# Kernel optimization log

Measured on AMD Instinct MI355X. Metric: run time of the kernel, lower is better.

Reference implementation:

```python
import jax, jax.numpy as jnp
import numpy as np

N = 50000      # nodes
E = 800000     # edges (before self loops)
G = 64         # graphs in batch
IN = 128       # in_features
HID = 64       # hidden_dim per head
HEADS = 4
NC = 2         # num_classes
SLOPE = 0.2    # PyG GATConv negative_slope default


def setup_inputs() -> dict:
    key = jax.random.key(0)
    ks = jax.random.split(key, 16)
    s = 0.1
    HC = HID * HEADS
    inp = {
        "x": jax.random.normal(ks[0], (N, IN), jnp.float32),
        "edge_index": jax.random.randint(ks[1], (2, E), 0, N, jnp.int64),
        "batch": jnp.sort(jax.random.randint(ks[2], (N,), 0, G, jnp.int64)),
        # GATConv 1: lin weight [H*C, IN], att vecs [H, C], bias [H*C]
        "W1": jax.random.normal(ks[3], (HC, IN), jnp.float32) * s,
        "as1": jax.random.normal(ks[4], (HEADS, HID), jnp.float32) * s,
        "ad1": jax.random.normal(ks[5], (HEADS, HID), jnp.float32) * s,
        "b1": jnp.zeros((HC,), jnp.float32),
        # GATConv 2
        "W2": jax.random.normal(ks[6], (HC, HC), jnp.float32) * s,
        "as2": jax.random.normal(ks[7], (HEADS, HID), jnp.float32) * s,
        "ad2": jax.random.normal(ks[8], (HEADS, HID), jnp.float32) * s,
        "b2": jnp.zeros((HC,), jnp.float32),
        # GATConv 3
        "W3": jax.random.normal(ks[9], (HC, HC), jnp.float32) * s,
        "as3": jax.random.normal(ks[10], (HEADS, HID), jnp.float32) * s,
        "ad3": jax.random.normal(ks[11], (HEADS, HID), jnp.float32) * s,
        "b3": jnp.zeros((HC,), jnp.float32),
        # MLP head
        "fc1_w": jax.random.normal(ks[12], (HID, HC), jnp.float32) * s,
        "fc1_b": jnp.zeros((HID,), jnp.float32),
        "fc2_w": jax.random.normal(ks[13], (NC, HID), jnp.float32) * s,
        "fc2_b": jnp.zeros((NC,), jnp.float32),
    }
    return inp


def gat_conv(x, src, dst, W, a_src, a_dst, b):
    """PyG-style GATConv (concat=True, self loops already in src/dst)."""
    n = x.shape[0]
    h = (x @ W.T).reshape(n, HEADS, HID)            # [N,H,C]
    al_s = jnp.sum(h * a_src[None], axis=-1)        # [N,H]
    al_d = jnp.sum(h * a_dst[None], axis=-1)        # [N,H]
    e = jax.nn.leaky_relu(al_s[src] + al_d[dst], SLOPE)  # [Et,H]
    # segment softmax over edges grouped by destination node
    m = jax.ops.segment_max(e, dst, num_segments=n)      # [N,H]
    ex = jnp.exp(e - m[dst])
    den = jax.ops.segment_sum(ex, dst, num_segments=n)
    alpha = ex / (den[dst] + 1e-16)                      # [Et,H]
    out = jax.ops.segment_sum(h[src] * alpha[:, :, None], dst, num_segments=n)
    return out.reshape(n, HEADS * HID) + b


def reference(x, edge_index, batch, W1, as1, ad1, b1, W2, as2, ad2, b2,
              W3, as3, ad3, b3, fc1_w, fc1_b, fc2_w, fc2_b):
    loops = jnp.arange(N, dtype=edge_index.dtype)
    src = jnp.concatenate([edge_index[0], loops])   # add_self_loops=True
    dst = jnp.concatenate([edge_index[1], loops])

    h = jax.nn.relu(gat_conv(x, src, dst, W1, as1, ad1, b1))
    h = jax.nn.relu(gat_conv(h, src, dst, W2, as2, ad2, b2))
    h = gat_conv(h, src, dst, W3, as3, ad3, b3)

    # global_mean_pool over batch vector
    sums = jax.ops.segment_sum(h, batch, num_segments=G)          # [G,H*C]
    cnts = jax.ops.segment_sum(jnp.ones((N,), h.dtype), batch, num_segments=G)
    pooled = sums / jnp.maximum(cnts, 1.0)[:, None]

    z = jax.nn.relu(pooled @ fc1_w.T + fc1_b)
    return z @ fc2_w.T + fc2_b                                    # [G,NC]
```

## Files before the change

### kernel.cpp

```cpp
#include <hip/hip_runtime.h>
#include <hip/hip_bf16.h>

#define N_NODES 50000
#define E_EDGES 800000
#define ET (E_EDGES + N_NODES)
#define G_GRAPHS 64
#define IN_F 128
#define HID 64
#define HEADS 4
#define HC (HID * HEADS)
#define NC 2
#define SLOPE 0.2f
#define L2E 1.4426950408889634f

typedef float f32x4 __attribute__((ext_vector_type(4)));
typedef __bf16 bf16x8 __attribute__((ext_vector_type(8)));
typedef unsigned short us8 __attribute__((ext_vector_type(8)));
typedef unsigned short us4 __attribute__((ext_vector_type(4)));
typedef _Float16 h16x4 __attribute__((ext_vector_type(4)));

#define MFMA16(a, b, c) \
  __builtin_amdgcn_mfma_f32_16x16x32_bf16(__builtin_bit_cast(bf16x8, (a)), \
                                          __builtin_bit_cast(bf16x8, (b)), (c), 0, 0, 0)

typedef __attribute__((address_space(1))) void gvoid;
typedef __attribute__((address_space(3))) void lvoid;
#define GLD16(g, l) \
  __builtin_amdgcn_global_load_lds((gvoid*)(g), (lvoid*)(l), 16, 0, 0)

__device__ inline unsigned short f2bf_rne(float f) {
  unsigned u = __builtin_bit_cast(unsigned, f);
  u += 0x7fffu + ((u >> 16) & 1u);
  return (unsigned short)(u >> 16);
}
__device__ inline float bf2f(unsigned short h) {
  unsigned u = ((unsigned)h) << 16;
  return __builtin_bit_cast(float, u);
}


__device__ inline void split4(const float* __restrict__ in, unsigned short* __restrict__ hi,
                              unsigned short* __restrict__ lo, int i) {
  float4 v = *(const float4*)&in[i];
  float f[4] = {v.x, v.y, v.z, v.w};
  us4 h, l;
#pragma unroll
  for (int j = 0; j < 4; j++) {
    unsigned short hb = f2bf_rne(f[j]);
    h[j] = hb;
    l[j] = f2bf_rne(f[j] - bf2f(hb));
  }
  *(us4*)&hi[i] = h;
  *(us4*)&lo[i] = l;
}

#define QX (N_NODES * IN_F / 4)
#define QW1 (HC * IN_F / 4)
#define QW2 (HC * HC / 4)
#define QTOT (QX + QW1 + 2 * QW2)

__global__ __launch_bounds__(256) void split_all_kernel(
    const float* __restrict__ x, const float* __restrict__ W1,
    const float* __restrict__ W2, const float* __restrict__ W3,
    unsigned short* __restrict__ xhi,
    unsigned short* __restrict__ w1h, unsigned short* __restrict__ w1l,
    unsigned short* __restrict__ w2h, unsigned short* __restrict__ w2l,
    unsigned short* __restrict__ w3h, unsigned short* __restrict__ w3l) {
  int q = blockIdx.x * 256 + threadIdx.x;
  if (q < QX) {
    int i = q * 4;
    float4 v = *(const float4*)&x[i];
    float f[4] = {v.x, v.y, v.z, v.w};
    us4 h;
#pragma unroll
    for (int j = 0; j < 4; j++) h[j] = f2bf_rne(f[j]);
    *(us4*)&xhi[i] = h;
  } else if (q < QX + QW1) {
    split4(W1, w1h, w1l, (q - QX) * 4);
  } else if (q < QX + QW1 + QW2) {
    split4(W2, w2h, w2l, (q - QX - QW1) * 4);
  } else {
    split4(W3, w3h, w3l, (q - QX - QW1 - QW2) * 4);
  }
}


__global__ void count_kernel(const int* __restrict__ ei, int* __restrict__ cnt) {
  int e = blockIdx.x * blockDim.x + threadIdx.x;
  if (e >= ET) return;
  int dst = (e < E_EDGES) ? ei[E_EDGES + e] : (e - E_EDGES);
  atomicAdd(&cnt[dst], 1);
}

#define SCAN_BLOCKS ((N_NODES + 255) / 256)

__global__ __launch_bounds__(256) void scan1_kernel(const int* __restrict__ cnt,
                                                    int* __restrict__ incl_buf,
                                                    int* __restrict__ partial) {
  __shared__ int ws[4];
  int tid = threadIdx.x, b = blockIdx.x;
  int wave = tid >> 6, lane = tid & 63;
  int i = b * 256 + tid;
  int v = (i < N_NODES) ? cnt[i] : 0;
  int x = v;
#pragma unroll
  for (int off = 1; off < 64; off <<= 1) {
    int t = __shfl_up(x, off, 64);
    if (lane >= off) x += t;
  }
  if (lane == 63) ws[wave] = x;
  __syncthreads();
  if (tid == 0) {
    int s = 0;
#pragma unroll
    for (int w = 0; w < 4; w++) { int t = ws[w]; ws[w] = s; s += t; }
    partial[b] = s;
  }
  __syncthreads();
  if (i < N_NODES) incl_buf[i] = x + ws[wave];
}

__global__ __launch_bounds__(256) void scan2_kernel(int* __restrict__ partial) {
  __shared__ int ws[4];
  int tid = threadIdx.x;
  int wave = tid >> 6, lane = tid & 63;
  int v = (tid < SCAN_BLOCKS) ? partial[tid] : 0;
  int x = v;
#pragma unroll
  for (int off = 1; off < 64; off <<= 1) {
    int t = __shfl_up(x, off, 64);
    if (lane >= off) x += t;
  }
  if (lane == 63) ws[wave] = x;
  __syncthreads();
  if (tid == 0) {
    int s = 0;
#pragma unroll
    for (int w = 0; w < 4; w++) { int t = ws[w]; ws[w] = s; s += t; }
  }
  __syncthreads();
  partial[tid] = x + ws[wave] - v;
}

__global__ __launch_bounds__(256) void scan3_kernel(const int* __restrict__ cnt,
                                                    int* __restrict__ incl_buf,
                                                    const int* __restrict__ partial,
                                                    int* __restrict__ rowptr,
                                                    int* __restrict__ cursor) {
  int tid = threadIdx.x, b = blockIdx.x;
  int i = b * 256 + tid;
  if (i >= N_NODES) return;
  int incl = incl_buf[i] + partial[b];
  rowptr[i + 1] = incl;
  cursor[i] = incl - cnt[i];
  if (i == 0) rowptr[0] = 0;
}

__global__ void scatter_kernel(const int* __restrict__ ei, int* __restrict__ cursor,
                               int* __restrict__ csr_src) {
  int e = blockIdx.x * blockDim.x + threadIdx.x;
  if (e >= ET) return;
  int src, dst;
  if (e < E_EDGES) { src = ei[e]; dst = ei[E_EDGES + e]; }
  else { src = e - E_EDGES; dst = src; }
  int pos = atomicAdd(&cursor[dst], 1);
  csr_src[pos] = src;
}


template <int K>
__global__ __launch_bounds__(256) void mfma_gemm_kernel(
    const unsigned short* __restrict__ A,
    const unsigned short* __restrict__ Whi, const unsigned short* __restrict__ Wlo,
    const float* __restrict__ a_s, const float* __restrict__ a_d,
    _Float16* __restrict__ hbuf16, float* __restrict__ als, float* __restrict__ ald) {
  __shared__ unsigned short As[4 * 64 * 8];
  __shared__ unsigned short Bs[2 * 4 * 256 * 8];

  int t = threadIdx.x;
  int mt = blockIdx.x;
  int w = t >> 6, lane = t & 63, lr = lane & 15, kg = lane >> 4;

  f32x4 acc[4][4];
#pragma unroll
  for (int m = 0; m < 4; m++)
#pragma unroll
    for (int nf = 0; nf < 4; nf++) {
      f32x4 z = {0.f, 0.f, 0.f, 0.f};
      acc[m][nf] = z;
    }

  for (int k0 = 0; k0 < K; k0 += 32) {
    __syncthreads();
#pragma unroll
    for (int j = 0; j < 8; j++) {
      int c = w * 512 + j * 64 + lane;
      int plane = c >> 10;
      int bkg = (c >> 8) & 3;
      int n = c & 255;
      const unsigned short* gsrc =
          (plane ? Wlo : Whi) + (size_t)n * K + k0 + bkg * 8;
      GLD16(gsrc, &Bs[(size_t)(w * 512 + j * 64) * 8]);
    }
    {
      const unsigned short* gsrc = A + (size_t)(mt * 64 + lane) * K + k0 + w * 8;
      GLD16(gsrc, &As[(size_t)(w * 64) * 8]);
    }
    __syncthreads();

    us8 bh[4], bl[4];
#pragma unroll
    for (int nf = 0; nf < 4; nf++) {
      int n = w * 64 + nf * 16 + lr;
      bh[nf] = *(us8*)&Bs[(size_t)(kg * 256 + n) * 8];
      bl[nf] = *(us8*)&Bs[(size_t)((4 + kg) * 256 + n) * 8];
    }
#pragma unroll
    for (int m = 0; m < 4; m++) {
      int row = m * 16 + lr;
      us8 ah = *(us8*)&As[(size_t)(kg * 64 + row) * 8];
#pragma unroll
      for (int nf = 0; nf < 4; nf++) {
        acc[m][nf] = MFMA16(ah, bh[nf], acc[m][nf]);
        acc[m][nf] = MFMA16(ah, bl[nf], acc[m][nf]);
      }
    }
  }

  int head = w;
  float asv[4], adv[4];
#pragma unroll
  for (int nf = 0; nf < 4; nf++) {
    asv[nf] = a_s[head * HID + nf * 16 + lr];
    adv[nf] = a_d[head * HID + nf * 16 + lr];
  }
#pragma unroll
  for (int m = 0; m < 4; m++) {
#pragma unroll
    for (int r = 0; r < 4; r++) {
      int grow = mt * 64 + m * 16 + kg * 4 + r;
      float ps = 0.f, pd = 0.f;
#pragma unroll
      for (int nf = 0; nf < 4; nf++) {
        float v = acc[m][nf][r];
        ps += v * asv[nf];
        pd += v * adv[nf];
        if (grow < N_NODES)
          hbuf16[(size_t)grow * HC + head * 64 + nf * 16 + lr] = (_Float16)v;
      }
#pragma unroll
      for (int msk = 1; msk < 16; msk <<= 1) {
        ps += __shfl_xor(ps, msk, 64);
        pd += __shfl_xor(pd, msk, 64);
      }
      if (lr == 0 && grow < N_NODES) {
        als[grow * HEADS + head] = ps * L2E;
        ald[grow * HEADS + head] = pd * L2E;
      }
    }
  }
}


template <int MODE>
__global__ __launch_bounds__(256) void agg_kernel(
    const _Float16* __restrict__ hbuf16, const float* __restrict__ alsE,
    const float* __restrict__ aldE, const int* __restrict__ rowptr,
    const int* __restrict__ csr_src, const float* __restrict__ bias,
    unsigned short* __restrict__ ohi, float* __restrict__ pooled,
    const int* __restrict__ batch) {
  int wave = threadIdx.x >> 6;
  int lane = threadIdx.x & 63;
  int v0 = blockIdx.x * 8 + wave * 2;
  int v1 = v0 + 1;
  int head = lane >> 4;
  float ald0 = aldE[(unsigned)v0 * HEADS + head];
  float ald1 = aldE[(unsigned)v1 * HEADS + head];
  int beg0 = rowptr[v0], n0 = rowptr[v0 + 1] - beg0;
  int beg1 = rowptr[v1], n1 = rowptr[v1 + 1] - beg1;
  int n = max(n0, n1);

  float den0 = 0.f, den1 = 0.f;
  f32x4 acc0 = {0.f, 0.f, 0.f, 0.f};
  f32x4 acc1 = {0.f, 0.f, 0.f, 0.f};
  const _Float16* hp = hbuf16 + (lane << 2);
#pragma unroll 2
  for (int i = 0; i < n; i++) {
    int s0 = csr_src[beg0 + min(i, n0 - 1)];
    int s1 = csr_src[beg1 + min(i, n1 - 1)];
    float a0 = alsE[(unsigned)s0 * HEADS + head] + ald0;
    float a1 = alsE[(unsigned)s1 * HEADS + head] + ald1;
    a0 = fmaxf(a0, SLOPE * a0);
    a1 = fmaxf(a1, SLOPE * a1);
    float ex0 = (i < n0) ? __builtin_amdgcn_exp2f(a0) : 0.f;
    float ex1 = (i < n1) ? __builtin_amdgcn_exp2f(a1) : 0.f;
    h16x4 h0 = *(const h16x4*)(hp + ((unsigned)s0 << 8));
    h16x4 h1 = *(const h16x4*)(hp + ((unsigned)s1 << 8));
    den0 += ex0; den1 += ex1;
    acc0[0] += (float)h0[0] * ex0; acc0[1] += (float)h0[1] * ex0;
    acc0[2] += (float)h0[2] * ex0; acc0[3] += (float)h0[3] * ex0;
    acc1[0] += (float)h1[0] * ex1; acc1[1] += (float)h1[1] * ex1;
    acc1[2] += (float)h1[2] * ex1; acc1[3] += (float)h1[3] * ex1;
  }
  float inv0 = 1.0f / (den0 + 1e-16f);
  float inv1 = 1.0f / (den1 + 1e-16f);
  float4 bv = *(const float4*)&bias[lane * 4];
  float o0[4], o1[4];
  o0[0] = acc0[0] * inv0 + bv.x; o0[1] = acc0[1] * inv0 + bv.y;
  o0[2] = acc0[2] * inv0 + bv.z; o0[3] = acc0[3] * inv0 + bv.w;
  o1[0] = acc1[0] * inv1 + bv.x; o1[1] = acc1[1] * inv1 + bv.y;
  o1[2] = acc1[2] * inv1 + bv.z; o1[3] = acc1[3] * inv1 + bv.w;

  if (MODE == 0) {
    us4 h0, h1;
#pragma unroll
    for (int j = 0; j < 4; j++) {
      h0[j] = f2bf_rne(fmaxf(o0[j], 0.f));
      h1[j] = f2bf_rne(fmaxf(o1[j], 0.f));
    }
    *(us4*)&ohi[(size_t)v0 * HC + lane * 4] = h0;
    *(us4*)&ohi[(size_t)v1 * HC + lane * 4] = h1;
  } else {
    __shared__ float pacc[8][HC];
    __shared__ int pg[8];
    f32x4 ov0 = {o0[0], o0[1], o0[2], o0[3]};
    f32x4 ov1 = {o1[0], o1[1], o1[2], o1[3]};
    *(f32x4*)&pacc[wave * 2][lane * 4] = ov0;
    *(f32x4*)&pacc[wave * 2 + 1][lane * 4] = ov1;
    if (lane == 0) {
      pg[wave * 2] = batch[v0];
      pg[wave * 2 + 1] = batch[v1];
    }
    __syncthreads();
    int c = threadIdx.x;
    float s = pacc[0][c];
    int gcur = pg[0];
#pragma unroll
    for (int wv = 1; wv < 8; wv++) {
      if (pg[wv] != gcur) {
        atomicAdd(&pooled[gcur * HC + c], s);
        s = 0.f;
        gcur = pg[wv];
      }
      s += pacc[wv][c];
    }
    atomicAdd(&pooled[gcur * HC + c], s);
  }
}


__global__ __launch_bounds__(64) void mlp_kernel(const float* __restrict__ pooled_sum,
                                                 const int* __restrict__ batch,
                                                 const float* __restrict__ w1,
                                                 const float* __restrict__ b1,
                                                 const float* __restrict__ w2,
                                                 const float* __restrict__ b2,
                                                 float* __restrict__ out) {
  int g = blockIdx.x;
  int j = threadIdx.x;
  int lo = 0, hi = N_NODES;
  while (lo < hi) { int mid = (lo + hi) >> 1; if (batch[mid] < g) lo = mid + 1; else hi = mid; }
  int start = lo;
  hi = N_NODES;
  while (lo < hi) { int mid = (lo + hi) >> 1; if (batch[mid] < g + 1) lo = mid + 1; else hi = mid; }
  float invc = 1.0f / fmaxf((float)(lo - start), 1.0f);
  __shared__ float z[HID];
  float acc = 0.f;
  for (int k = 0; k < HC; k++) acc += pooled_sum[g * HC + k] * w1[j * HC + k];
  z[j] = fmaxf(acc * invc + b1[j], 0.f);
  __syncthreads();
  if (j < NC) {
    float o = b2[j];
    for (int k = 0; k < HID; k++) o += z[k] * w2[j * HID + k];
    out[g * NC + j] = o;
  }
}


extern "C" void kernel_launch(void* const* d_in, const int* in_sizes, int n_in,
                              void* d_out, int out_size, void* d_ws, size_t ws_size,
                              hipStream_t stream) {
  const float* x    = (const float*)d_in[0];
  const int*   ei   = (const int*)d_in[1];
  const int*   batch= (const int*)d_in[2];
  const float* W1   = (const float*)d_in[3];
  const float* as1  = (const float*)d_in[4];
  const float* ad1  = (const float*)d_in[5];
  const float* b1   = (const float*)d_in[6];
  const float* W2   = (const float*)d_in[7];
  const float* as2  = (const float*)d_in[8];
  const float* ad2  = (const float*)d_in[9];
  const float* b2   = (const float*)d_in[10];
  const float* W3   = (const float*)d_in[11];
  const float* as3  = (const float*)d_in[12];
  const float* ad3  = (const float*)d_in[13];
  const float* b3   = (const float*)d_in[14];
  const float* fc1w = (const float*)d_in[15];
  const float* fc1b = (const float*)d_in[16];
  const float* fc2w = (const float*)d_in[17];
  const float* fc2b = (const float*)d_in[18];
  float* out = (float*)d_out;

  char* ws = (char*)d_ws;
  size_t off = 0;
  _Float16* hbuf16 = (_Float16*)(ws + off); off += (size_t)N_NODES * HC * 2;
  unsigned short* ahi = (unsigned short*)(ws + off); off += (size_t)N_NODES * HC * 2;
  unsigned short* xhi = (unsigned short*)(ws + off); off += (size_t)N_NODES * IN_F * 2;
  unsigned short* w1h = (unsigned short*)(ws + off); off += (size_t)HC * IN_F * 2;
  unsigned short* w1l = (unsigned short*)(ws + off); off += (size_t)HC * IN_F * 2;
  unsigned short* w2h = (unsigned short*)(ws + off); off += (size_t)HC * HC * 2;
  unsigned short* w2l = (unsigned short*)(ws + off); off += (size_t)HC * HC * 2;
  unsigned short* w3h = (unsigned short*)(ws + off); off += (size_t)HC * HC * 2;
  unsigned short* w3l = (unsigned short*)(ws + off); off += (size_t)HC * HC * 2;
  float* als    = (float*)(ws + off); off += (size_t)N_NODES * HEADS * 4;
  float* ald    = (float*)(ws + off); off += (size_t)N_NODES * HEADS * 4;
  float* pooled = (float*)(ws + off); off += (size_t)G_GRAPHS * HC * 4;
  int*   cnt    = (int*)(ws + off);   off += (size_t)N_NODES * 4;
  int*   cursor = (int*)(ws + off);   off += (size_t)N_NODES * 4;
  int*   csrsrc = (int*)(ws + off);   off += (size_t)ET * 4;
  int*   rowptr = (int*)(ws + off);   off += (size_t)(N_NODES + 1) * 4;
  int*   partial= (int*)(ws + off);   off += 256 * 4;

  split_all_kernel<<<(QTOT + 255) / 256, 256, 0, stream>>>(
      x, W1, W2, W3, xhi, w1h, w1l, w2h, w2l, w3h, w3l);

  hipMemsetAsync(cnt, 0, (size_t)N_NODES * 4, stream);
  hipMemsetAsync(pooled, 0, (size_t)G_GRAPHS * HC * 4, stream);
  count_kernel<<<(ET + 255) / 256, 256, 0, stream>>>(ei, cnt);
  scan1_kernel<<<SCAN_BLOCKS, 256, 0, stream>>>(cnt, cursor, partial);
  scan2_kernel<<<1, 256, 0, stream>>>(partial);
  scan3_kernel<<<SCAN_BLOCKS, 256, 0, stream>>>(cnt, cursor, partial, rowptr, cursor);
  scatter_kernel<<<(ET + 255) / 256, 256, 0, stream>>>(ei, cursor, csrsrc);

  dim3 gemm_grid((N_NODES + 63) / 64);
  int agg_grid = N_NODES / 8;

  mfma_gemm_kernel<IN_F><<<gemm_grid, 256, 0, stream>>>(xhi, w1h, w1l, as1, ad1, hbuf16, als, ald);
  agg_kernel<0><<<agg_grid, 256, 0, stream>>>(hbuf16, als, ald, rowptr, csrsrc, b1, ahi, nullptr, nullptr);
  mfma_gemm_kernel<HC><<<gemm_grid, 256, 0, stream>>>(ahi, w2h, w2l, as2, ad2, hbuf16, als, ald);
  agg_kernel<0><<<agg_grid, 256, 0, stream>>>(hbuf16, als, ald, rowptr, csrsrc, b2, ahi, nullptr, nullptr);
  mfma_gemm_kernel<HC><<<gemm_grid, 256, 0, stream>>>(ahi, w3h, w3l, as3, ad3, hbuf16, als, ald);
  agg_kernel<1><<<agg_grid, 256, 0, stream>>>(hbuf16, als, ald, rowptr, csrsrc, b3, nullptr, pooled, batch);

  mlp_kernel<<<G_GRAPHS, 64, 0, stream>>>(pooled, batch, fc1w, fc1b, fc2w, fc2b, out);
}
```

Measured before the change: 457.8 us.

## Load GEMM operands directly from global into registers with double buffering

Removes the LDS staging (global_load_lds plus two barriers per k-step) in the MFMA GEMM. Each lane now loads its A and W fragments straight from global memory into a two-deep register buffer, prefetching the next k-slice while the current one feeds the MFMAs. This drops the synchronisation and LDS traffic but makes each wave fetch W separately, with no sharing through shared memory, and raises register pressure. Row indices are also clamped to stay within bounds.

```diff
diff --git a/kernel.cpp b/kernel.cpp
--- a/kernel.cpp
+++ b/kernel.cpp
@@ -22,11 +22,6 @@
 #define MFMA16(a, b, c) \
   __builtin_amdgcn_mfma_f32_16x16x32_bf16(__builtin_bit_cast(bf16x8, (a)), \
                                           __builtin_bit_cast(bf16x8, (b)), (c), 0, 0, 0)
-
-typedef __attribute__((address_space(1))) void gvoid;
-typedef __attribute__((address_space(3))) void lvoid;
-#define GLD16(g, l) \
-  __builtin_amdgcn_global_load_lds((gvoid*)(g), (lvoid*)(l), 16, 0, 0)
 
 __device__ inline unsigned short f2bf_rne(float f) {
   unsigned u = __builtin_bit_cast(unsigned, f);
@@ -174,9 +169,6 @@
     const unsigned short* __restrict__ Whi, const unsigned short* __restrict__ Wlo,
     const float* __restrict__ a_s, const float* __restrict__ a_d,
     _Float16* __restrict__ hbuf16, float* __restrict__ als, float* __restrict__ ald) {
-  __shared__ unsigned short As[4 * 64 * 8];
-  __shared__ unsigned short Bs[2 * 4 * 256 * 8];
-
   int t = threadIdx.x;
   int mt = blockIdx.x;
   int w = t >> 6, lane = t & 63, lr = lane & 15, kg = lane >> 4;
@@ -190,39 +182,49 @@
       acc[m][nf] = z;
     }
 
+  const unsigned short* ap[4];
+#pragma unroll
+  for (int m = 0; m < 4; m++) {
+    int row = min(mt * 64 + m * 16 + lr, N_NODES - 1);
+    ap[m] = A + (size_t)row * K + kg * 8;
+  }
+  const unsigned short *bph[4], *bpl[4];
+#pragma unroll
+  for (int nf = 0; nf < 4; nf++) {
+    int n = w * 64 + nf * 16 + lr;
+    bph[nf] = Whi + (size_t)n * K + kg * 8;
+    bpl[nf] = Wlo + (size_t)n * K + kg * 8;
+  }
+
+  us8 af[2][4], bh[2][4], bl[2][4];
+#pragma unroll
+  for (int m = 0; m < 4; m++) af[0][m] = *(const us8*)ap[m];
+#pragma unroll
+  for (int nf = 0; nf < 4; nf++) {
+    bh[0][nf] = *(const us8*)bph[nf];
+    bl[0][nf] = *(const us8*)bpl[nf];
+  }
+
+#pragma unroll
   for (int k0 = 0; k0 < K; k0 += 32) {
-    __syncthreads();
-#pragma unroll
-    for (int j = 0; j < 8; j++) {
-      int c = w * 512 + j * 64 + lane;
-      int plane = c >> 10;
-      int bkg = (c >> 8) & 3;
-      int n = c & 255;
-      const unsigned short* gsrc =
-          (plane ? Wlo : Whi) + (size_t)n * K + k0 + bkg * 8;
-      GLD16(gsrc, &Bs[(size_t)(w * 512 + j * 64) * 8]);
-    }
-    {
-      const unsigned short* gsrc = A + (size_t)(mt * 64 + lane) * K + k0 + w * 8;
-      GLD16(gsrc, &As[(size_t)(w * 64) * 8]);
-    }
-    __syncthreads();
-
-    us8 bh[4], bl[4];
-#pragma unroll
-    for (int nf = 0; nf < 4; nf++) {
-      int n = w * 64 + nf * 16 + lr;
-      bh[nf] = *(us8*)&Bs[(size_t)(kg * 256 + n) * 8];
-      bl[nf] = *(us8*)&Bs[(size_t)((4 + kg) * 256 + n) * 8];
+    const int buf = (k0 >> 5) & 1;
+    const int nbuf = buf ^ 1;
+    if (k0 + 32 < K) {
+      int k1 = k0 + 32;
+#pragma unroll
+      for (int m = 0; m < 4; m++) af[nbuf][m] = *(const us8*)(ap[m] + k1);
+#pragma unroll
+      for (int nf = 0; nf < 4; nf++) {
+        bh[nbuf][nf] = *(const us8*)(bph[nf] + k1);
+        bl[nbuf][nf] = *(const us8*)(bpl[nf] + k1);
+      }
     }
 #pragma unroll
     for (int m = 0; m < 4; m++) {
-      int row = m * 16 + lr;
-      us8 ah = *(us8*)&As[(size_t)(kg * 64 + row) * 8];
 #pragma unroll
       for (int nf = 0; nf < 4; nf++) {
-        acc[m][nf] = MFMA16(ah, bh[nf], acc[m][nf]);
-        acc[m][nf] = MFMA16(ah, bl[nf], acc[m][nf]);
+        acc[m][nf] = MFMA16(af[buf][m], bh[buf][nf], acc[m][nf]);
+        acc[m][nf] = MFMA16(af[buf][m], bl[buf][nf], acc[m][nf]);
       }
     }
   }
```

Measured after the change: 469.0 us. 2.5% more time.
